# Kernel optimization log

Hardware: AMD Instinct MI355X
Metric: run time of the kernel (lower is better)

Reference implementation:

```python
import jax, jax.numpy as jnp
import numpy as np

N = 100000          # total nodes
E = 1600000         # total edges
B = 500             # graphs in batch
NODES_PER_GRAPH = N // B
D_X, D_XDA = 96, 32
IN = D_X + D_XDA    # 128
HID = 128
OUT = 128


def setup_inputs() -> dict:
    key = jax.random.key(0)
    ks = jax.random.split(key, 12)
    s = 0.05
    x = jax.random.normal(ks[0], (N, D_X), jnp.float32)
    x_da = jax.random.normal(ks[1], (N, D_XDA), jnp.float32)
    edge_index = jax.random.randint(ks[2], (2, E), 0, N, jnp.int32).astype(jnp.int64)
    batch = (jnp.arange(N, dtype=jnp.int64) // NODES_PER_GRAPH)
    rootindex = jnp.arange(B, dtype=jnp.int64) * NODES_PER_GRAPH
    return {
        'x': x, 'x_da': x_da, 'edge_index': edge_index,
        'batch': batch, 'rootindex': rootindex,
        'td_w1': jax.random.normal(ks[3], (IN, HID), jnp.float32) * s,
        'td_b1': jnp.zeros((HID,), jnp.float32),
        'td_w2': jax.random.normal(ks[4], (HID + IN, OUT), jnp.float32) * s,
        'td_b2': jnp.zeros((OUT,), jnp.float32),
        'bu_w1': jax.random.normal(ks[5], (IN, HID), jnp.float32) * s,
        'bu_b1': jnp.zeros((HID,), jnp.float32),
        'bu_w2': jax.random.normal(ks[6], (HID + IN, OUT), jnp.float32) * s,
        'bu_b2': jnp.zeros((OUT,), jnp.float32),
        'mlp_w1': jax.random.normal(ks[7], ((OUT + HID) * 2, 2 * HID), jnp.float32) * s,
        'mlp_b1': jnp.zeros((2 * HID,), jnp.float32),
        'mlp_w2': jax.random.normal(ks[8], (2 * HID, 2), jnp.float32) * s,
        'mlp_b2': jnp.zeros((2,), jnp.float32),
    }


def gcn_conv(h, src, dst, W, b):
    # PyG GCNConv: h' = D^{-1/2} (A + I) D^{-1/2} (h W) + b,
    # messages flow src -> dst, deg counts incoming edges + self loop.
    h = h @ W                                              # [N, out]
    deg = jax.ops.segment_sum(jnp.ones((src.shape[0],), h.dtype), dst,
                              num_segments=N) + 1.0        # self loop
    dinv = jax.lax.rsqrt(deg)                              # deg >= 1
    norm = dinv[src] * dinv[dst]                           # [E]
    agg = jax.ops.segment_sum(h[src] * norm[:, None], dst, num_segments=N)
    agg = agg + h * (dinv * dinv)[:, None]                 # self-loop term
    return agg + b


def branch(x0, src, dst, w1, b1, w2, b2, batch, rootindex):
    # x0: [N, IN] = cat(x, x_da)
    x1 = x0
    h = gcn_conv(x0, src, dst, w1, b1)                     # [N, HID]
    x2 = h
    root1 = x1[rootindex[batch]]                           # root-extend gather
    h = jax.nn.relu(jnp.concatenate([h, root1], axis=1))   # dropout off (eval)
    h = jax.nn.relu(gcn_conv(h, src, dst, w2, b2))         # [N, OUT]
    root2 = x2[rootindex[batch]]
    h = jnp.concatenate([h, root2], axis=1)                # [N, OUT+HID]
    # scatter_mean over graphs
    sums = jax.ops.segment_sum(h, batch, num_segments=B)
    cnt = jax.ops.segment_sum(jnp.ones((N,), h.dtype), batch, num_segments=B)
    return sums / cnt[:, None]                             # [B, OUT+HID]


def reference(x, x_da, edge_index, batch, rootindex,
              td_w1, td_b1, td_w2, td_b2,
              bu_w1, bu_b1, bu_w2, bu_b2,
              mlp_w1, mlp_b1, mlp_w2, mlp_b2):
    x0 = jnp.concatenate([x, x_da], axis=1)                # [N, IN]
    src, dst = edge_index[0], edge_index[1]
    td = branch(x0, src, dst, td_w1, td_b1, td_w2, td_b2, batch, rootindex)
    bu = branch(x0, dst, src, bu_w1, bu_b1, bu_w2, bu_b2, batch, rootindex)
    g = jnp.concatenate([bu, td], axis=1)                  # [B, 4*HID]
    h = jax.nn.relu(g @ mlp_w1 + mlp_b1)
    return h @ mlp_w2 + mlp_b2                             # [B, 2]
```

## Files before the change

### kernel.cpp

```cpp
#include <hip/hip_runtime.h>

#define NN 100000
#define NE 1600000
#define NB 500
#define NPG 200
#define BS 256
#define NBUK 391
#define SLAB 4608
#define EPB4 4096
#define NEB4 391
#define NBLK 1563

typedef unsigned short ushortT;
typedef __attribute__((ext_vector_type(8))) short bf16x8;
typedef __attribute__((ext_vector_type(4))) float f32x4;

#define MFMA16(a, b, c) __builtin_amdgcn_mfma_f32_16x16x32_bf16(a, b, c, 0, 0, 0)

__device__ inline ushortT f2bf(float f) {
    unsigned u = __float_as_uint(f);
    return (ushortT)((u + 0x7FFF + ((u >> 16) & 1)) >> 16);
}
__device__ inline float bf2f(ushortT u) { return __uint_as_float((unsigned)u << 16); }
__device__ inline float4 bf4_to_f4(ushort4 u) {
    return make_float4(bf2f(u.x), bf2f(u.y), bf2f(u.z), bf2f(u.w));
}
__device__ inline bf16x8 cvt8(float4 f0, float4 f1) {
    bf16x8 r;
    r[0] = (short)f2bf(f0.x); r[1] = (short)f2bf(f0.y);
    r[2] = (short)f2bf(f0.z); r[3] = (short)f2bf(f0.w);
    r[4] = (short)f2bf(f1.x); r[5] = (short)f2bf(f1.y);
    r[6] = (short)f2bf(f1.z); r[7] = (short)f2bf(f1.w);
    return r;
}
__device__ inline bf16x8 relu_bf8(uint4 w) {
    bf16x8 r;
    unsigned ws[4] = {w.x, w.y, w.z, w.w};
#pragma unroll
    for (int i = 0; i < 4; i++) {
        unsigned v = ws[i];
        unsigned lo = (v & 0x8000u) ? 0u : (v & 0xFFFFu);
        unsigned hi = (v & 0x80000000u) ? 0u : (v & 0xFFFF0000u);
        r[2 * i]     = (short)lo;
        r[2 * i + 1] = (short)(hi >> 16);
    }
    return r;
}

__global__ void wprep_k(const float* __restrict__ w0, const float* __restrict__ w1,
                        const float* __restrict__ w2, const float* __restrict__ w3,
                        ushortT* __restrict__ wt, int* __restrict__ bcnt) {
    if (blockIdx.x == 0) {
        for (int i = threadIdx.x; i < 2 * NBUK; i += 256) bcnt[i] = 0;
    }
    int m = blockIdx.x >> 6;
    const float* w = (m == 0) ? w0 : (m == 1) ? w1 : (m == 2) ? w2 : w3;
    ushortT* o = wt + m * 16384;
    int idx = (blockIdx.x & 63) * 256 + threadIdx.x;
    int n = idx >> 7, k = idx & 127;
    o[idx] = f2bf(w[k * 128 + n]);
}

__global__ __launch_bounds__(256) void phase1_k(
    const int* __restrict__ ei,
    int* __restrict__ bcnt_td, int* __restrict__ bcnt_bu,
    int* __restrict__ st_td, int* __restrict__ st_bu,
    const float* __restrict__ x, const float* __restrict__ xda,
    const ushortT* __restrict__ WTa, const ushortT* __restrict__ WTb,
    ushortT* __restrict__ hs_a, ushortT* __restrict__ hs_b,
    const int* __restrict__ root,
    const float* __restrict__ W2a, const float* __restrict__ W2b,
    float* __restrict__ rm_a, float* __restrict__ rm_b) {
    const int t = threadIdx.x;
    if (blockIdx.x < NEB4) {
        __shared__ int h0[NBUK], h1[NBUK];
        for (int i = t; i < NBUK; i += 256) { h0[i] = 0; h1[i] = 0; }
        __syncthreads();
        int base = blockIdx.x * EPB4;
        int a[16], b[16];
#pragma unroll
        for (int j = 0; j < 16; j++) {
            int e = base + t + j * 256;
            a[j] = -1;
            if (e < NE) {
                a[j] = ei[e]; b[j] = ei[NE + e];
                atomicAdd(&h0[b[j] >> 8], 1);
                atomicAdd(&h1[a[j] >> 8], 1);
            }
        }
        __syncthreads();
        for (int i = t; i < NBUK; i += 256) {
            int c0 = h0[i], c1 = h1[i];
            if (c0) h0[i] = atomicAdd(&bcnt_td[i], c0);
            if (c1) h1[i] = atomicAdd(&bcnt_bu[i], c1);
        }
        __syncthreads();
#pragma unroll
        for (int j = 0; j < 16; j++) {
            if (a[j] >= 0) {
                int bk0 = b[j] >> 8;
                int o0 = atomicAdd(&h0[bk0], 1);
                st_td[bk0 * SLAB + o0] = (a[j] << 8) | (b[j] & 255);
                int bk1 = a[j] >> 8;
                int o1 = atomicAdd(&h1[bk1], 1);
                st_bu[bk1 * SLAB + o1] = (b[j] << 8) | (a[j] & 255);
            }
        }
        return;
    }
    if (blockIdx.x >= NEB4 + NBLK) {
        int b = blockIdx.x - NEB4 - NBLK;
        __shared__ float xr[128];
        int r = root[b];
        if (t < 128) {
            float val = (t < 96) ? x[(size_t)r * 96 + t] : xda[(size_t)r * 32 + (t - 96)];
            xr[t] = fmaxf(val, 0.f);
        }
        __syncthreads();
        int br = t >> 7, c = t & 127;
        const float* W2 = br ? W2b : W2a;
        float* rm = br ? rm_b : rm_a;
        float acc = 0.f;
#pragma unroll 8
        for (int k = 0; k < 128; k++)
            acc = fmaf(xr[k], W2[(size_t)(128 + k) * 128 + c], acc);
        rm[(size_t)b * 128 + c] = acc;
        return;
    }
    const int blk = blockIdx.x - NEB4;
    const int wv = t >> 6, l = t & 63, lr = l & 15, lk = l >> 4;
    const int row0 = blk * 64;
    const int cb0 = (wv * 2) * 16, cb1 = (wv * 2 + 1) * 16;

    bf16x8 bfr[2][2][4];
#pragma unroll
    for (int br = 0; br < 2; br++) {
        const ushortT* WT = br ? WTb : WTa;
#pragma unroll
        for (int c = 0; c < 2; c++) {
            const ushortT* base = WT + (size_t)((wv * 2 + c) * 16 + lr) * 128 + lk * 8;
#pragma unroll
            for (int kk = 0; kk < 4; kk++)
                bfr[br][c][kk] = *reinterpret_cast<const bf16x8*>(base + kk * 32);
        }
    }

#pragma unroll
    for (int rt = 0; rt < 4; rt++) {
        const int rtbase = row0 + rt * 16;
        int arow = rtbase + lr; if (arow >= NN) arow = NN - 1;
        bf16x8 af[4];
#pragma unroll
        for (int kk = 0; kk < 4; kk++) {
            int c8 = kk * 4 + lk;
            float4 f0, f1;
            if (c8 < 12) {
                const float* p = x + (size_t)arow * 96 + c8 * 8;
                f0 = *(const float4*)p; f1 = *(const float4*)(p + 4);
            } else {
                const float* p = xda + (size_t)arow * 32 + (c8 - 12) * 8;
                f0 = *(const float4*)p; f1 = *(const float4*)(p + 4);
            }
            af[kk] = cvt8(f0, f1);
        }
        f32x4 a00 = {0,0,0,0}, a01 = {0,0,0,0}, a10 = {0,0,0,0}, a11 = {0,0,0,0};
#pragma unroll
        for (int kk = 0; kk < 4; kk++) {
            a00 = MFMA16(af[kk], bfr[0][0][kk], a00);
            a01 = MFMA16(af[kk], bfr[0][1][kk], a01);
            a10 = MFMA16(af[kk], bfr[1][0][kk], a10);
            a11 = MFMA16(af[kk], bfr[1][1][kk], a11);
        }
        const int srow = rtbase + lk * 4;
#pragma unroll
        for (int e = 0; e < 4; e++) {
            int r = srow + e;
            if (r < NN) {
                size_t ro = (size_t)r * 128;
                hs_a[ro + cb0 + lr] = f2bf(a00[e]);
                hs_a[ro + cb1 + lr] = f2bf(a01[e]);
                hs_b[ro + cb0 + lr] = f2bf(a10[e]);
                hs_b[ro + cb1 + lr] = f2bf(a11[e]);
            }
        }
    }
}

__global__ __launch_bounds__(256) void place2_k(
    const int* __restrict__ st_td, const int* __restrict__ st_bu,
    const int* __restrict__ bcnt_td, const int* __restrict__ bcnt_bu,
    int* __restrict__ rp_td, int* __restrict__ rp_bu,
    int* __restrict__ csr_td, int* __restrict__ csr_bu,
    float* __restrict__ dinv_td, float* __restrict__ dinv_bu) {
    const int dir = blockIdx.x >= NBUK;
    const int bucket = dir ? blockIdx.x - NBUK : blockIdx.x;
    const int* stage = (dir ? st_bu : st_td) + bucket * SLAB;
    const int* bcnt = dir ? bcnt_bu : bcnt_td;
    const int n = bcnt[bucket];
    int* rp = dir ? rp_bu : rp_td;
    int* csr = dir ? csr_bu : csr_td;
    float* dinv = dir ? dinv_bu : dinv_td;
    const int t = threadIdx.x;

    __shared__ int rw[4];
    __shared__ int sh_obase;
    int part = 0;
    for (int i = t; i < bucket; i += 256) part += bcnt[i];
#pragma unroll
    for (int off = 32; off; off >>= 1) part += __shfl_down(part, off);
    if ((t & 63) == 0) rw[t >> 6] = part;
    __syncthreads();
    if (t == 0) sh_obase = rw[0] + rw[1] + rw[2] + rw[3];
    __syncthreads();
    const int obase = sh_obase;

    const int node0 = bucket << 8;
    __shared__ int lcnt[BS], lsc[BS], lcur[BS];
    lcnt[t] = 0;
    __syncthreads();
    for (int i = t; i < n; i += 256) atomicAdd(&lcnt[stage[i] & 255], 1);
    __syncthreads();
    lsc[t] = lcnt[t];
    __syncthreads();
#pragma unroll
    for (int off = 1; off < BS; off <<= 1) {
        int add = (t >= off) ? lsc[t - off] : 0;
        __syncthreads();
        lsc[t] += add;
        __syncthreads();
    }
    {
        int excl = lsc[t] - lcnt[t];
        lcur[t] = obase + excl;
        int node = node0 + t;
        if (node < NN) {
            rp[node] = obase + excl;
            dinv[node] = rsqrtf((float)(lcnt[t] + 1));
        }
    }
    if (bucket == NBUK - 1 && t == 0) rp[NN] = obase + n;
    __syncthreads();
    for (int i = t; i < n; i += 256) {
        int s = stage[i];
        int off = atomicAdd(&lcur[s & 255], 1);
        csr[off] = (int)((unsigned)s >> 8);
    }
}

__global__ __launch_bounds__(256) void gemm2x_k(
    const ushortT* __restrict__ agg_a, const ushortT* __restrict__ agg_b,
    const ushortT* __restrict__ WTa, const ushortT* __restrict__ WTb,
    const float* __restrict__ rm_a, const float* __restrict__ rm_b,
    const float* __restrict__ dinv_a, const float* __restrict__ dinv_b,
    const int* __restrict__ root, float* __restrict__ x2a, float* __restrict__ x2b,
    ushortT* __restrict__ hs_a, ushortT* __restrict__ hs_b) {
    const int t = threadIdx.x;
    if (blockIdx.x >= 2 * NBLK) {
        int b = blockIdx.x - 2 * NBLK;
        int br = t >> 7, c = t & 127;
        const ushortT* agg = br ? agg_b : agg_a;
        float* x2 = br ? x2b : x2a;
        int r = root[b];
        x2[(size_t)b * 128 + c] = bf2f(agg[(size_t)r * 128 + c]);
        return;
    }
    const int brn = blockIdx.x >= NBLK;
    const ushortT* agg = brn ? agg_b : agg_a;
    const ushortT* WT  = brn ? WTb : WTa;
    const float* rm    = brn ? rm_b : rm_a;
    const float* dinv  = brn ? dinv_b : dinv_a;
    ushortT* hs        = brn ? hs_b : hs_a;
    const int blk = brn ? blockIdx.x - NBLK : blockIdx.x;
    const int wv = t >> 6, l = t & 63, lr = l & 15, lk = l >> 4;
    const int row0 = blk * 64;
    const int cb0 = (wv * 2) * 16, cb1 = (wv * 2 + 1) * 16;

    bf16x8 bfr[2][4];
#pragma unroll
    for (int c = 0; c < 2; c++) {
        const ushortT* base = WT + (size_t)((wv * 2 + c) * 16 + lr) * 128 + lk * 8;
#pragma unroll
        for (int kk = 0; kk < 4; kk++)
            bfr[c][kk] = *reinterpret_cast<const bf16x8*>(base + kk * 32);
    }

#pragma unroll
    for (int rt = 0; rt < 4; rt++) {
        const int rtbase = row0 + rt * 16;
        int arow = rtbase + lr; if (arow >= NN) arow = NN - 1;
        const ushortT* ap = agg + (size_t)arow * 128 + lk * 8;
        bf16x8 af[4];
#pragma unroll
        for (int kk = 0; kk < 4; kk++)
            af[kk] = relu_bf8(*reinterpret_cast<const uint4*>(ap + kk * 32));
        f32x4 a0 = {0,0,0,0}, a1 = {0,0,0,0};
#pragma unroll
        for (int kk = 0; kk < 4; kk++) {
            a0 = MFMA16(af[kk], bfr[0][kk], a0);
            a1 = MFMA16(af[kk], bfr[1][kk], a1);
        }
        const int srow = rtbase + lk * 4;
        float4 dv = *(const float4*)(dinv + srow);
        const float* dvp = (const float*)&dv;
#pragma unroll
        for (int e = 0; e < 4; e++) {
            int r = srow + e;
            if (r < NN) {
                int bg = r / NPG;
                size_t ro = (size_t)r * 128;
                float r0 = rm[(size_t)bg * 128 + cb0 + lr];
                float r1 = rm[(size_t)bg * 128 + cb1 + lr];
                hs[ro + cb0 + lr] = f2bf((a0[e] + r0) * dvp[e]);
                hs[ro + cb1 + lr] = f2bf((a1[e] + r1) * dvp[e]);
            }
        }
    }
}

template <int MODE, int EDGE_DINV>
__global__ __launch_bounds__(256) void gather2x_k(
    const int* __restrict__ rp_a, const int* __restrict__ csr_a,
    const float* __restrict__ dinv_a, const ushortT* __restrict__ hs_a,
    const float* __restrict__ bias_a,
    const int* __restrict__ rp_b, const int* __restrict__ csr_b,
    const float* __restrict__ dinv_b, const ushortT* __restrict__ hs_b,
    const float* __restrict__ bias_b,
    ushortT* __restrict__ out_a, ushortT* __restrict__ out_b) {
    int v = blockIdx.x * 8 + (threadIdx.x >> 5);
    if (v >= NN) return;
    const int lane = threadIdx.x & 31;
    int ba = rp_a[v], ea = rp_a[v + 1];
    int bb = rp_b[v], eb = rp_b[v + 1];
    float dva = dinv_a[v], dvb = dinv_b[v];
    float4 acc_a, acc_b;
    {
        float4 fs = bf4_to_f4(((const ushort4*)(hs_a + (size_t)v * 128))[lane]);
        float sa = EDGE_DINV ? dva : 1.f;
        acc_a = make_float4(fs.x * sa, fs.y * sa, fs.z * sa, fs.w * sa);
        fs = bf4_to_f4(((const ushort4*)(hs_b + (size_t)v * 128))[lane]);
        float sb = EDGE_DINV ? dvb : 1.f;
        acc_b = make_float4(fs.x * sb, fs.y * sb, fs.z * sb, fs.w * sb);
    }

    while (ba < ea || bb < eb) {
        int na = ea - ba; if (na > 32) na = 32; if (na < 0) na = 0;
        int nb = eb - bb; if (nb > 32) nb = 32; if (nb < 0) nb = 0;
        int ia = (lane < na) ? csr_a[ba + lane] : 0;
        int ib = (lane < nb) ? csr_b[bb + lane] : 0;
        float fa = 1.f, fb = 1.f;
        if (EDGE_DINV) { fa = dinv_a[ia]; fb = dinv_b[ib]; }
        for (int i = 0; i < 32; i += 8) {
            if (i >= na && i >= nb) break;
            ushort4 ua[8], ub[8];
            float da8[8], db8[8];
            if (i < na) {
#pragma unroll
                for (int j = 0; j < 8; j++) {
                    int s = __shfl(ia, i + j, 32);
                    if (EDGE_DINV) da8[j] = __shfl(fa, i + j, 32);
                    ua[j] = ((const ushort4*)(hs_a + (size_t)s * 128))[lane];
                }
            }
            if (i < nb) {
#pragma unroll
                for (int j = 0; j < 8; j++) {
                    int s = __shfl(ib, i + j, 32);
                    if (EDGE_DINV) db8[j] = __shfl(fb, i + j, 32);
                    ub[j] = ((const ushort4*)(hs_b + (size_t)s * 128))[lane];
                }
            }
            if (i < na) {
#pragma unroll
                for (int j = 0; j < 8; j++)
                    if (i + j < na) {
                        float4 f = bf4_to_f4(ua[j]);
                        if (EDGE_DINV) {
                            acc_a.x = fmaf(f.x, da8[j], acc_a.x);
                            acc_a.y = fmaf(f.y, da8[j], acc_a.y);
                            acc_a.z = fmaf(f.z, da8[j], acc_a.z);
                            acc_a.w = fmaf(f.w, da8[j], acc_a.w);
                        } else {
                            acc_a.x += f.x; acc_a.y += f.y; acc_a.z += f.z; acc_a.w += f.w;
                        }
                    }
            }
            if (i < nb) {
#pragma unroll
                for (int j = 0; j < 8; j++)
                    if (i + j < nb) {
                        float4 f = bf4_to_f4(ub[j]);
                        if (EDGE_DINV) {
                            acc_b.x = fmaf(f.x, db8[j], acc_b.x);
                            acc_b.y = fmaf(f.y, db8[j], acc_b.y);
                            acc_b.z = fmaf(f.z, db8[j], acc_b.z);
                            acc_b.w = fmaf(f.w, db8[j], acc_b.w);
                        } else {
                            acc_b.x += f.x; acc_b.y += f.y; acc_b.z += f.z; acc_b.w += f.w;
                        }
                    }
            }
        }
        ba += 32; bb += 32;
    }

    float4 pa = ((const float4*)bias_a)[lane];
    float4 pb = ((const float4*)bias_b)[lane];
    float4 oa = make_float4(fmaf(acc_a.x, dva, pa.x), fmaf(acc_a.y, dva, pa.y),
                            fmaf(acc_a.z, dva, pa.z), fmaf(acc_a.w, dva, pa.w));
    float4 ob = make_float4(fmaf(acc_b.x, dvb, pb.x), fmaf(acc_b.y, dvb, pb.y),
                            fmaf(acc_b.z, dvb, pb.z), fmaf(acc_b.w, dvb, pb.w));
    if (MODE == 1) {
        oa.x = fmaxf(oa.x, 0.f); oa.y = fmaxf(oa.y, 0.f); oa.z = fmaxf(oa.z, 0.f); oa.w = fmaxf(oa.w, 0.f);
        ob.x = fmaxf(ob.x, 0.f); ob.y = fmaxf(ob.y, 0.f); ob.z = fmaxf(ob.z, 0.f); ob.w = fmaxf(ob.w, 0.f);
    }
    ((ushort4*)(out_a + (size_t)v * 128))[lane] =
        make_ushort4(f2bf(oa.x), f2bf(oa.y), f2bf(oa.z), f2bf(oa.w));
    ((ushort4*)(out_b + (size_t)v * 128))[lane] =
        make_ushort4(f2bf(ob.x), f2bf(ob.y), f2bf(ob.z), f2bf(ob.w));
}

__global__ __launch_bounds__(256) void mlp_k(
    const ushortT* __restrict__ ra, const ushortT* __restrict__ rb,
    const float* __restrict__ x2a, const float* __restrict__ x2b,
    const float* __restrict__ w1, const float* __restrict__ b1,
    const float* __restrict__ w2, const float* __restrict__ b2,
    float* __restrict__ out) {
    __shared__ float gs[512];
    __shared__ float parts[4][2];
    int b = blockIdx.x, t = threadIdx.x;
    int br = t >> 7, c = t & 127;
    {
        const ushortT* src = br ? rb : ra;
        size_t base = (size_t)b * NPG * 128 + c;
        float s = 0.f;
#pragma unroll 4
        for (int r = 0; r < NPG; r++)
            s += bf2f(src[base + (size_t)r * 128]);
        const float* x2 = br ? x2b : x2a;
        gs[br * 256 + c]       = s * (1.0f / NPG);
        gs[br * 256 + 128 + c] = x2[(size_t)b * 128 + c];
    }
    __syncthreads();
    float acc = b1[t];
#pragma unroll 8
    for (int k = 0; k < 512; k++)
        acc = fmaf(gs[k], w1[(size_t)k * 256 + t], acc);
    float hv = fmaxf(acc, 0.f);
    float p0 = hv * w2[t * 2 + 0];
    float p1 = hv * w2[t * 2 + 1];
#pragma unroll
    for (int off = 32; off; off >>= 1) {
        p0 += __shfl_down(p0, off);
        p1 += __shfl_down(p1, off);
    }
    int w = t >> 6;
    if ((t & 63) == 0) { parts[w][0] = p0; parts[w][1] = p1; }
    __syncthreads();
    if (t == 0) {
        out[b * 2 + 0] = parts[0][0] + parts[1][0] + parts[2][0] + parts[3][0] + b2[0];
        out[b * 2 + 1] = parts[0][1] + parts[1][1] + parts[2][1] + parts[3][1] + b2[1];
    }
}

extern "C" void kernel_launch(void* const* d_in, const int* in_sizes, int n_in,
                              void* d_out, int out_size, void* d_ws, size_t ws_size,
                              hipStream_t stream) {
    const float* x     = (const float*)d_in[0];
    const float* xda   = (const float*)d_in[1];
    const int*   ei    = (const int*)d_in[2];
    const int*   root  = (const int*)d_in[4];
    const float* td_w1 = (const float*)d_in[5];
    const float* td_b1 = (const float*)d_in[6];
    const float* td_w2 = (const float*)d_in[7];
    const float* td_b2 = (const float*)d_in[8];
    const float* bu_w1 = (const float*)d_in[9];
    const float* bu_b1 = (const float*)d_in[10];
    const float* bu_w2 = (const float*)d_in[11];
    const float* bu_b2 = (const float*)d_in[12];
    const float* mw1   = (const float*)d_in[13];
    const float* mb1   = (const float*)d_in[14];
    const float* mw2   = (const float*)d_in[15];
    const float* mb2   = (const float*)d_in[16];
    float* out = (float*)d_out;

    ushortT* agg_bu  = (ushortT*)d_ws;
    ushortT* agg_td  = agg_bu + (size_t)NN * 128;
    ushortT* hs_bu   = agg_td + (size_t)NN * 128;
    ushortT* hs_td   = hs_bu + (size_t)NN * 128;
    float*   dinv_td = (float*)(hs_td + (size_t)NN * 128);
    float*   dinv_bu = dinv_td + NN;
    float*   x2_bu   = dinv_bu + NN;
    float*   x2_td   = x2_bu + (size_t)NB * 128;
    float*   rm_bu   = x2_td + (size_t)NB * 128;
    float*   rm_td   = rm_bu + (size_t)NB * 128;
    ushortT* wt1_bu  = (ushortT*)(rm_td + (size_t)NB * 128);
    ushortT* wt1_td  = wt1_bu + 16384;
    ushortT* wt2_bu  = wt1_td + 16384;
    ushortT* wt2_td  = wt2_bu + 16384;
    int*     bcnt_td = (int*)(wt2_td + 16384);
    int*     bcnt_bu = bcnt_td + NBUK;
    int*     rp_td   = bcnt_bu + NBUK;
    int*     rp_bu   = rp_td + NN + 1;
    int*     csr_td  = rp_bu + NN + 1;
    int*     csr_bu  = csr_td + NE;
    int*     st_td   = (int*)agg_bu;
    int*     st_bu   = st_td + NBUK * SLAB;

    wprep_k<<<4 * 64, 256, 0, stream>>>(bu_w1, td_w1, bu_w2, td_w2, wt1_bu, bcnt_td);

    phase1_k<<<NEB4 + NBLK + NB, 256, 0, stream>>>(
        ei, bcnt_td, bcnt_bu, st_td, st_bu,
        x, xda, wt1_bu, wt1_td, hs_bu, hs_td,
        root, bu_w2, td_w2, rm_bu, rm_td);

    place2_k<<<2 * NBUK, 256, 0, stream>>>(st_td, st_bu, bcnt_td, bcnt_bu,
                                           rp_td, rp_bu, csr_td, csr_bu,
                                           dinv_td, dinv_bu);

    gather2x_k<0, 1><<<(NN + 7) / 8, 256, 0, stream>>>(
        rp_bu, csr_bu, dinv_bu, hs_bu, bu_b1,
        rp_td, csr_td, dinv_td, hs_td, td_b1, agg_bu, agg_td);

    gemm2x_k<<<2 * NBLK + NB, 256, 0, stream>>>(
        agg_bu, agg_td, wt2_bu, wt2_td, rm_bu, rm_td,
        dinv_bu, dinv_td, root, x2_bu, x2_td, hs_bu, hs_td);

    gather2x_k<1, 0><<<(NN + 7) / 8, 256, 0, stream>>>(
        rp_bu, csr_bu, dinv_bu, hs_bu, bu_b2,
        rp_td, csr_td, dinv_td, hs_td, td_b2, agg_bu, agg_td);

    mlp_k<<<NB, 256, 0, stream>>>(agg_bu, agg_td, x2_bu, x2_td,
                                  mw1, mb1, mw2, mb2, out);
}
```

Before: 442.8 us.

## Split gather into per-branch column-sliced kernels with 8-lane node groups

Replaces the fused dual-branch gather, which used 32 lanes per node loading 8 bytes each, with a per-branch kernel. It splits the 128 feature columns into 8 slices of 16, and each block handles 32 nodes with 8 lanes loading 4 bytes per neighbor. The block index interleaves slices so that concurrent blocks work on the same column slice, aiming for better L2 locality of the random neighbor rows and less wasted lane work for short adjacency lists. The cost is that CSR indices and dinv values are re-read for every slice, each load is narrower, and the kernel launch count doubles.

Measured after the change: 968.6 us. 119% more time.

```diff
diff --git a/kernel.cpp b/kernel.cpp
--- a/kernel.cpp
+++ b/kernel.cpp
@@ -10,6 +10,7 @@
 #define EPB4 4096
 #define NEB4 391
 #define NBLK 1563
+#define NGCHUNK 3125
 
 typedef unsigned short ushortT;
 typedef __attribute__((ext_vector_type(8))) short bf16x8;
@@ -22,9 +23,6 @@
     return (ushortT)((u + 0x7FFF + ((u >> 16) & 1)) >> 16);
 }
 __device__ inline float bf2f(ushortT u) { return __uint_as_float((unsigned)u << 16); }
-__device__ inline float4 bf4_to_f4(ushort4 u) {
-    return make_float4(bf2f(u.x), bf2f(u.y), bf2f(u.z), bf2f(u.w));
-}
 __device__ inline bf16x8 cvt8(float4 f0, float4 f1) {
     bf16x8 r;
     r[0] = (short)f2bf(f0.x); r[1] = (short)f2bf(f0.y);
@@ -318,105 +316,52 @@
 }
 
 template <int MODE, int EDGE_DINV>
-__global__ __launch_bounds__(256) void gather2x_k(
-    const int* __restrict__ rp_a, const int* __restrict__ csr_a,
-    const float* __restrict__ dinv_a, const ushortT* __restrict__ hs_a,
-    const float* __restrict__ bias_a,
-    const int* __restrict__ rp_b, const int* __restrict__ csr_b,
-    const float* __restrict__ dinv_b, const ushortT* __restrict__ hs_b,
-    const float* __restrict__ bias_b,
-    ushortT* __restrict__ out_a, ushortT* __restrict__ out_b) {
-    int v = blockIdx.x * 8 + (threadIdx.x >> 5);
-    if (v >= NN) return;
-    const int lane = threadIdx.x & 31;
-    int ba = rp_a[v], ea = rp_a[v + 1];
-    int bb = rp_b[v], eb = rp_b[v + 1];
-    float dva = dinv_a[v], dvb = dinv_b[v];
-    float4 acc_a, acc_b;
+__global__ __launch_bounds__(256) void gatherS_k(
+    const int* __restrict__ rp, const int* __restrict__ csr,
+    const float* __restrict__ dinv, const ushortT* __restrict__ hs,
+    const float* __restrict__ bias, ushortT* __restrict__ outp) {
+    const int slice = blockIdx.x & 7;
+    const int chunk = blockIdx.x >> 3;
+    const int g = threadIdx.x >> 3;
+    const int lane = threadIdx.x & 7;
+    const int v = chunk * 32 + g;
+    const int coff = slice * 16 + lane * 2;
+
+    int beg = rp[v], end = rp[v + 1];
+    float dv = dinv[v];
+    float ax, ay;
     {
-        float4 fs = bf4_to_f4(((const ushort4*)(hs_a + (size_t)v * 128))[lane]);
-        float sa = EDGE_DINV ? dva : 1.f;
-        acc_a = make_float4(fs.x * sa, fs.y * sa, fs.z * sa, fs.w * sa);
-        fs = bf4_to_f4(((const ushort4*)(hs_b + (size_t)v * 128))[lane]);
-        float sb = EDGE_DINV ? dvb : 1.f;
-        acc_b = make_float4(fs.x * sb, fs.y * sb, fs.z * sb, fs.w * sb);
-    }
-
-    while (ba < ea || bb < eb) {
-        int na = ea - ba; if (na > 32) na = 32; if (na < 0) na = 0;
-        int nb = eb - bb; if (nb > 32) nb = 32; if (nb < 0) nb = 0;
-        int ia = (lane < na) ? csr_a[ba + lane] : 0;
-        int ib = (lane < nb) ? csr_b[bb + lane] : 0;
-        float fa = 1.f, fb = 1.f;
-        if (EDGE_DINV) { fa = dinv_a[ia]; fb = dinv_b[ib]; }
-        for (int i = 0; i < 32; i += 8) {
-            if (i >= na && i >= nb) break;
-            ushort4 ua[8], ub[8];
-            float da8[8], db8[8];
-            if (i < na) {
-#pragma unroll
-                for (int j = 0; j < 8; j++) {
-                    int s = __shfl(ia, i + j, 32);
-                    if (EDGE_DINV) da8[j] = __shfl(fa, i + j, 32);
-                    ua[j] = ((const ushort4*)(hs_a + (size_t)s * 128))[lane];
-                }
-            }
-            if (i < nb) {
-#pragma unroll
-                for (int j = 0; j < 8; j++) {
-                    int s = __shfl(ib, i + j, 32);
-                    if (EDGE_DINV) db8[j] = __shfl(fb, i + j, 32);
-                    ub[j] = ((const ushort4*)(hs_b + (size_t)s * 128))[lane];
-                }
-            }
-            if (i < na) {
-#pragma unroll
-                for (int j = 0; j < 8; j++)
-                    if (i + j < na) {
-                        float4 f = bf4_to_f4(ua[j]);
-                        if (EDGE_DINV) {
-                            acc_a.x = fmaf(f.x, da8[j], acc_a.x);
-                            acc_a.y = fmaf(f.y, da8[j], acc_a.y);
-                            acc_a.z = fmaf(f.z, da8[j], acc_a.z);
-                            acc_a.w = fmaf(f.w, da8[j], acc_a.w);
-                        } else {
-                            acc_a.x += f.x; acc_a.y += f.y; acc_a.z += f.z; acc_a.w += f.w;
-                        }
-                    }
-            }
-            if (i < nb) {
-#pragma unroll
-                for (int j = 0; j < 8; j++)
-                    if (i + j < nb) {
-                        float4 f = bf4_to_f4(ub[j]);
-                        if (EDGE_DINV) {
-                            acc_b.x = fmaf(f.x, db8[j], acc_b.x);
-                            acc_b.y = fmaf(f.y, db8[j], acc_b.y);
-                            acc_b.z = fmaf(f.z, db8[j], acc_b.z);
-                            acc_b.w = fmaf(f.w, db8[j], acc_b.w);
-                        } else {
-                            acc_b.x += f.x; acc_b.y += f.y; acc_b.z += f.z; acc_b.w += f.w;
-                        }
-                    }
-            }
-        }
-        ba += 32; bb += 32;
-    }
-
-    float4 pa = ((const float4*)bias_a)[lane];
-    float4 pb = ((const float4*)bias_b)[lane];
-    float4 oa = make_float4(fmaf(acc_a.x, dva, pa.x), fmaf(acc_a.y, dva, pa.y),
-                            fmaf(acc_a.z, dva, pa.z), fmaf(acc_a.w, dva, pa.w));
-    float4 ob = make_float4(fmaf(acc_b.x, dvb, pb.x), fmaf(acc_b.y, dvb, pb.y),
-                            fmaf(acc_b.z, dvb, pb.z), fmaf(acc_b.w, dvb, pb.w));
-    if (MODE == 1) {
-        oa.x = fmaxf(oa.x, 0.f); oa.y = fmaxf(oa.y, 0.f); oa.z = fmaxf(oa.z, 0.f); oa.w = fmaxf(oa.w, 0.f);
-        ob.x = fmaxf(ob.x, 0.f); ob.y = fmaxf(ob.y, 0.f); ob.z = fmaxf(ob.z, 0.f); ob.w = fmaxf(ob.w, 0.f);
-    }
-    ((ushort4*)(out_a + (size_t)v * 128))[lane] =
-        make_ushort4(f2bf(oa.x), f2bf(oa.y), f2bf(oa.z), f2bf(oa.w));
-    ((ushort4*)(out_b + (size_t)v * 128))[lane] =
-        make_ushort4(f2bf(ob.x), f2bf(ob.y), f2bf(ob.z), f2bf(ob.w));
+        unsigned w = *(const unsigned*)(hs + (size_t)v * 128 + coff);
+        float sa = EDGE_DINV ? dv : 1.f;
+        ax = __uint_as_float(w << 16) * sa;
+        ay = __uint_as_float(w & 0xFFFF0000u) * sa;
+    }
+    for (int base = beg; base < end; base += 8) {
+        int n = end - base; if (n > 8) n = 8;
+        int idx = (lane < n) ? csr[base + lane] : 0;
+        float fd = EDGE_DINV ? dinv[idx] : 1.f;
+        unsigned w8[8];
+        float f8[8];
+#pragma unroll
+        for (int j = 0; j < 8; j++) {
+            int s = __shfl(idx, j, 8);
+            if (EDGE_DINV) f8[j] = __shfl(fd, j, 8);
+            w8[j] = *(const unsigned*)(hs + (size_t)s * 128 + coff);
+        }
+#pragma unroll
+        for (int j = 0; j < 8; j++) {
+            if (j < n) {
+                float lo = __uint_as_float(w8[j] << 16);
+                float hi = __uint_as_float(w8[j] & 0xFFFF0000u);
+                if (EDGE_DINV) { ax = fmaf(lo, f8[j], ax); ay = fmaf(hi, f8[j], ay); }
+                else           { ax += lo; ay += hi; }
+            }
+        }
+    }
+    float bx = bias[coff], by = bias[coff + 1];
+    float ox = fmaf(ax, dv, bx), oy = fmaf(ay, dv, by);
+    if (MODE == 1) { ox = fmaxf(ox, 0.f); oy = fmaxf(oy, 0.f); }
+    *(ushort2*)(outp + (size_t)v * 128 + coff) = make_ushort2(f2bf(ox), f2bf(oy));
 }
 
 __global__ __launch_bounds__(256) void mlp_k(
@@ -517,17 +462,15 @@
                                            rp_td, rp_bu, csr_td, csr_bu,
                                            dinv_td, dinv_bu);
 
-    gather2x_k<0, 1><<<(NN + 7) / 8, 256, 0, stream>>>(
-        rp_bu, csr_bu, dinv_bu, hs_bu, bu_b1,
-        rp_td, csr_td, dinv_td, hs_td, td_b1, agg_bu, agg_td);
+    gatherS_k<0, 1><<<8 * NGCHUNK, 256, 0, stream>>>(rp_bu, csr_bu, dinv_bu, hs_bu, bu_b1, agg_bu);
+    gatherS_k<0, 1><<<8 * NGCHUNK, 256, 0, stream>>>(rp_td, csr_td, dinv_td, hs_td, td_b1, agg_td);
 
     gemm2x_k<<<2 * NBLK + NB, 256, 0, stream>>>(
         agg_bu, agg_td, wt2_bu, wt2_td, rm_bu, rm_td,
         dinv_bu, dinv_td, root, x2_bu, x2_td, hs_bu, hs_td);
 
-    gather2x_k<1, 0><<<(NN + 7) / 8, 256, 0, stream>>>(
-        rp_bu, csr_bu, dinv_bu, hs_bu, bu_b2,
-        rp_td, csr_td, dinv_td, hs_td, td_b2, agg_bu, agg_td);
+    gatherS_k<1, 0><<<8 * NGCHUNK, 256, 0, stream>>>(rp_bu, csr_bu, dinv_bu, hs_bu, bu_b2, agg_bu);
+    gatherS_k<1, 0><<<8 * NGCHUNK, 256, 0, stream>>>(rp_td, csr_td, dinv_td, hs_td, td_b2, agg_td);
 
     mlp_k<<<NB, 256, 0, stream>>>(agg_bu, agg_td, x2_bu, x2_td,
                                   mw1, mb1, mw2, mb2, out);
```
